# Kernel optimization log

Hardware: AMD Instinct MI355X
Metric: run time of the kernel (lower is better)

The kernel has to match this reference:

```python
import jax, jax.numpy as jnp
import numpy as np

DIM = 4096
NUM_EXPERTS = 8
TOP_K = 2
TOKENS = 8192  # batch 2 * seq 4096


def setup_inputs() -> dict:
    key = jax.random.key(0)
    k1, k2 = jax.random.split(key)
    x = jax.random.normal(k1, (TOKENS, DIM), dtype=jnp.float32)
    W = jax.random.normal(k2, (NUM_EXPERTS, DIM), dtype=jnp.float32) * 0.02  # router weight, trunc-normal-ish
    return {"x": x, "W": W}


def reference(x, W):
    # Routing: linear -> top-k -> softmax over the k selected scores (fp32) -> cast back
    expert_scores = jnp.einsum("td,ed->te", x, W)                       # [T, E]
    top_scores, selected = jax.lax.top_k(expert_scores, TOP_K)          # [T, K], [T, K]
    top_scores = jax.nn.softmax(top_scores.astype(jnp.float32), axis=-1).astype(x.dtype)

    flat_expert_indices = selected.reshape(-1)                           # [T*K]
    # torch.histc(bins=E, min=0, max=E) on integer expert ids == bincount
    num_tokens_per_expert = jnp.bincount(flat_expert_indices, length=NUM_EXPERTS)

    # Stable argsort groups tokens by destination expert, preserving token order within an expert
    sorted_indices = jnp.argsort(flat_expert_indices, stable=True)       # [T*K]
    scatter_indices = sorted_indices // TOP_K                            # original token id per slot
    x_gathered = x[scatter_indices]                                      # [T*K, D]
    scores_sorted = top_scores.reshape(-1)[sorted_indices]               # [T*K]
    return x_gathered, num_tokens_per_expert, scatter_indices, scores_sorted
```

## Files before the change

### kernel.cpp

```cpp
#include <hip/hip_runtime.h>
#include <cstdint>

#define TOKENS 8192
#define DIM 4096
#define D4 (DIM / 4)
#define NEXP 8
#define TOPK 2
#define SLOTS (TOKENS * TOPK)

#define NBLK 512
#define TPB 256
#define TOK_PER_BLK 16
#define CH 32

#define OUT_CNT ((size_t)SLOTS * DIM)
#define OUT_SCAT (OUT_CNT + NEXP)
#define OUT_SCORE (OUT_SCAT + SLOTS)

typedef float vfloat4 __attribute__((ext_vector_type(4)));

__global__ __launch_bounds__(TPB, 2) void k_moe(const float* __restrict__ x,
                                                const float* __restrict__ W,
                                                int* __restrict__ hist,
                                                int* __restrict__ bar,
                                                float* __restrict__ out)
{
    __shared__ int   s_eid[CH];
    __shared__ float s_prob[CH];
    __shared__ int   s_cnt[NEXP];
    __shared__ int   s_pos[CH];

    const int wave = threadIdx.x >> 6;
    const int lane = threadIdx.x & 63;
    const int blk  = blockIdx.x;
    const int tok0 = (blk * 4 + wave) * 4;

    if (threadIdx.x < NEXP) s_cnt[threadIdx.x] = 0;
    __syncthreads();

    const float4* x4 = reinterpret_cast<const float4*>(x);
    const float4* W4 = reinterpret_cast<const float4*>(W);

    float acc[4][NEXP];
#pragma unroll
    for (int t = 0; t < 4; ++t)
#pragma unroll
        for (int e = 0; e < NEXP; ++e) acc[t][e] = 0.f;

    for (int i = 0; i < 16; ++i) {
        const int d4 = lane + 64 * i;
        float4 xv[4];
#pragma unroll
        for (int t = 0; t < 4; ++t) xv[t] = x4[(size_t)(tok0 + t) * D4 + d4];
#pragma unroll
        for (int e = 0; e < NEXP; ++e) {
            const float4 w = W4[e * D4 + d4];
#pragma unroll
            for (int t = 0; t < 4; ++t) {
                acc[t][e] = fmaf(xv[t].x, w.x, acc[t][e]);
                acc[t][e] = fmaf(xv[t].y, w.y, acc[t][e]);
                acc[t][e] = fmaf(xv[t].z, w.z, acc[t][e]);
                acc[t][e] = fmaf(xv[t].w, w.w, acc[t][e]);
            }
        }
    }

#pragma unroll
    for (int t = 0; t < 4; ++t)
#pragma unroll
        for (int e = 0; e < NEXP; ++e) {
            float v = acc[t][e];
#pragma unroll
            for (int off = 32; off >= 1; off >>= 1) v += __shfl_xor(v, off);
            acc[t][e] = v;
        }

#pragma unroll
    for (int t = 0; t < 4; ++t) {
        int i0 = 0;
        float m0 = acc[t][0];
#pragma unroll
        for (int e = 1; e < NEXP; ++e)
            if (acc[t][e] > m0) { m0 = acc[t][e]; i0 = e; }
        int i1 = -1;
        float m1 = -INFINITY;
#pragma unroll
        for (int e = 0; e < NEXP; ++e)
            if (e != i0 && acc[t][e] > m1) { m1 = acc[t][e]; i1 = e; }
        const float z = __expf(m1 - m0);
        const float inv = 1.0f / (1.0f + z);
        if (lane == t) {
            const int ls = (wave * 4 + t) * 2;
            s_eid[ls]      = i0;
            s_eid[ls + 1]  = i1;
            s_prob[ls]     = inv;
            s_prob[ls + 1] = z * inv;
            atomicAdd(&s_cnt[i0], 1);
            atomicAdd(&s_cnt[i1], 1);
        }
    }
    __syncthreads();
    if (threadIdx.x < NEXP) hist[blk * NEXP + threadIdx.x] = s_cnt[threadIdx.x];

    __syncthreads();
    if (threadIdx.x == 0) { __threadfence(); atomicAdd(&bar[0], 1); }

    if (blk == 0) {
        if (threadIdx.x == 0) {
            while (__hip_atomic_load(&bar[0], __ATOMIC_ACQUIRE,
                                     __HIP_MEMORY_SCOPE_AGENT) < NBLK)
                __builtin_amdgcn_s_sleep(2);
        }
        __syncthreads();
        if (threadIdx.x < 64) {
            int v[NEXP][8];
#pragma unroll
            for (int q = 0; q < NEXP; ++q)
#pragma unroll
                for (int r = 0; r < 8; ++r)
                    v[q][r] = hist[(r * 64 + lane) * NEXP + q];
            int base = 0;
#pragma unroll
            for (int q = 0; q < NEXP; ++q) {
                int run = 0;
#pragma unroll
                for (int r = 0; r < 8; ++r) {
                    int incl = v[q][r];
#pragma unroll
                    for (int off = 1; off <= 32; off <<= 1) {
                        const int n = __shfl_up(incl, off);
                        if (lane >= off) incl += n;
                    }
                    hist[(r * 64 + lane) * NEXP + q] = base + run + incl - v[q][r];
                    run += __shfl(incl, 63);
                }
                if (lane == 0) out[OUT_CNT + q] = (float)run;
                base += run;
            }
        }
    }

    __syncthreads();
    if (threadIdx.x == 0) {
        __threadfence();
        atomicAdd(&bar[32], 1);
        while (__hip_atomic_load(&bar[32], __ATOMIC_ACQUIRE,
                                 __HIP_MEMORY_SCOPE_AGENT) < NBLK)
            __builtin_amdgcn_s_sleep(2);
    }
    __syncthreads();

    if (threadIdx.x < 64) {
        const int e = (lane < CH) ? s_eid[lane] : -1;
        const unsigned long long lt = (1ull << lane) - 1ull;
        int rank = 0;
#pragma unroll
        for (int q = 0; q < NEXP; ++q) {
            const unsigned long long m = __ballot(e == q);
            if (e == q) rank = __popcll(m & lt);
        }
        if (lane < CH) {
            const int p = hist[blk * NEXP + e] + rank;
            s_pos[lane] = p;
            const int s = blk * CH + lane;
            out[OUT_SCAT + p]  = (float)(s >> 1);
            out[OUT_SCORE + p] = s_prob[lane];
        }
    }
    __syncthreads();

    const vfloat4* xx = reinterpret_cast<const vfloat4*>(x) +
                        (size_t)(blk * TOK_PER_BLK) * D4;
    vfloat4* o4 = reinterpret_cast<vfloat4*>(out);
#pragma unroll 2
    for (int tt = 0; tt < TOK_PER_BLK; ++tt) {
        const int p0 = s_pos[2 * tt];
        const int p1 = s_pos[2 * tt + 1];
        const vfloat4* src = xx + (size_t)tt * D4;
        vfloat4* d0 = o4 + (size_t)p0 * D4;
        vfloat4* d1 = o4 + (size_t)p1 * D4;
#pragma unroll
        for (int i = 0; i < 4; ++i) {
            const int idx = threadIdx.x + TPB * i;
            const vfloat4 v = src[idx];
            __builtin_nontemporal_store(v, d0 + idx);
            __builtin_nontemporal_store(v, d1 + idx);
        }
    }
}

extern "C" void kernel_launch(void* const* d_in, const int* in_sizes, int n_in,
                              void* d_out, int out_size, void* d_ws, size_t ws_size,
                              hipStream_t stream)
{
    const float* x = (const float*)d_in[0];
    const float* W = (const float*)d_in[1];
    float* out = (float*)d_out;

    int* hist = (int*)d_ws;
    int* bar  = (int*)((char*)d_ws + 64 * 1024);

    hipMemsetAsync(bar, 0, 256, stream);
    k_moe<<<NBLK, TPB, 0, stream>>>(x, W, hist, bar, out);
}
```

Before: 444.3 us.

## Split routing and gather into separate kernels with per-token gather blocks

The fused routing-plus-gather kernel is split in two. The routing kernel now writes each slot's destination position to a workspace array and exits. A second kernel, with one block per token, copies the x row to its two output rows using normal stores instead of nontemporal ones. This gives the bandwidth-bound copy far more parallelism than 512 blocks can offer, at the cost of one extra launch, a second read of x from L2 or HBM, and losing the nontemporal store hint. The dot-product loop in the routing kernel also gets an unroll-2 pragma.

```diff
diff --git a/kernel.cpp b/kernel.cpp
--- a/kernel.cpp
+++ b/kernel.cpp
@@ -10,7 +10,6 @@
 
 #define NBLK 512
 #define TPB 256
-#define TOK_PER_BLK 16
 #define CH 32
 
 #define OUT_CNT ((size_t)SLOTS * DIM)
@@ -19,16 +18,16 @@
 
 typedef float vfloat4 __attribute__((ext_vector_type(4)));
 
-__global__ __launch_bounds__(TPB, 2) void k_moe(const float* __restrict__ x,
-                                                const float* __restrict__ W,
-                                                int* __restrict__ hist,
-                                                int* __restrict__ bar,
-                                                float* __restrict__ out)
+__global__ __launch_bounds__(TPB, 2) void k_route(const float* __restrict__ x,
+                                                  const float* __restrict__ W,
+                                                  int* __restrict__ hist,
+                                                  int* __restrict__ bar,
+                                                  int* __restrict__ dstpos,
+                                                  float* __restrict__ out)
 {
     __shared__ int   s_eid[CH];
     __shared__ float s_prob[CH];
     __shared__ int   s_cnt[NEXP];
-    __shared__ int   s_pos[CH];
 
     const int wave = threadIdx.x >> 6;
     const int lane = threadIdx.x & 63;
@@ -47,6 +46,7 @@
 #pragma unroll
         for (int e = 0; e < NEXP; ++e) acc[t][e] = 0.f;
 
+#pragma unroll 2
     for (int i = 0; i < 16; ++i) {
         const int d4 = lane + 64 * i;
         float4 xv[4];
@@ -161,31 +161,31 @@
         }
         if (lane < CH) {
             const int p = hist[blk * NEXP + e] + rank;
-            s_pos[lane] = p;
             const int s = blk * CH + lane;
+            dstpos[s] = p;
             out[OUT_SCAT + p]  = (float)(s >> 1);
             out[OUT_SCORE + p] = s_prob[lane];
         }
     }
-    __syncthreads();
-
-    const vfloat4* xx = reinterpret_cast<const vfloat4*>(x) +
-                        (size_t)(blk * TOK_PER_BLK) * D4;
+}
+
+__global__ __launch_bounds__(TPB) void k_gather(const float* __restrict__ x,
+                                                const int* __restrict__ dstpos,
+                                                float* __restrict__ out)
+{
+    const int t = blockIdx.x;
+    const int p0 = dstpos[t * 2];
+    const int p1 = dstpos[t * 2 + 1];
+    const vfloat4* src = reinterpret_cast<const vfloat4*>(x) + (size_t)t * D4;
     vfloat4* o4 = reinterpret_cast<vfloat4*>(out);
-#pragma unroll 2
-    for (int tt = 0; tt < TOK_PER_BLK; ++tt) {
-        const int p0 = s_pos[2 * tt];
-        const int p1 = s_pos[2 * tt + 1];
-        const vfloat4* src = xx + (size_t)tt * D4;
-        vfloat4* d0 = o4 + (size_t)p0 * D4;
-        vfloat4* d1 = o4 + (size_t)p1 * D4;
-#pragma unroll
-        for (int i = 0; i < 4; ++i) {
-            const int idx = threadIdx.x + TPB * i;
-            const vfloat4 v = src[idx];
-            __builtin_nontemporal_store(v, d0 + idx);
-            __builtin_nontemporal_store(v, d1 + idx);
-        }
+    vfloat4* d0 = o4 + (size_t)p0 * D4;
+    vfloat4* d1 = o4 + (size_t)p1 * D4;
+#pragma unroll
+    for (int i = 0; i < 4; ++i) {
+        const int idx = threadIdx.x + TPB * i;
+        const vfloat4 v = src[idx];
+        d0[idx] = v;
+        d1[idx] = v;
     }
 }
 
@@ -197,9 +197,11 @@
     const float* W = (const float*)d_in[1];
     float* out = (float*)d_out;
 
-    int* hist = (int*)d_ws;
-    int* bar  = (int*)((char*)d_ws + 64 * 1024);
+    int* hist   = (int*)d_ws;
+    int* bar    = (int*)((char*)d_ws + 64 * 1024);
+    int* dstpos = (int*)((char*)d_ws + 128 * 1024);
 
     hipMemsetAsync(bar, 0, 256, stream);
-    k_moe<<<NBLK, TPB, 0, stream>>>(x, W, hist, bar, out);
+    k_route<<<NBLK, TPB, 0, stream>>>(x, W, hist, bar, dstpos, out);
+    k_gather<<<TOKENS, TPB, 0, stream>>>(x, dstpos, out);
 }
```

Result: slower. 454.3 us (+2.2%).
